# Kernel optimization log

Measured on AMD Instinct MI355X. Metric: run time of the kernel, lower is better.

The kernel has to match this reference:

```python
import jax, jax.numpy as jnp
import numpy as np

N, E, F_IN, H, C = 10000, 640000, 128, 128, 40


def setup_inputs() -> dict:
    key = jax.random.key(0)
    ks = jax.random.split(key, 8)
    x = jax.random.normal(ks[0], (N, F_IN), dtype=jnp.float32)
    edge_index = jax.random.randint(ks[1], (2, E), 0, N, dtype=jnp.int64)
    W1 = jax.random.normal(ks[2], (F_IN, H), dtype=jnp.float32) / np.sqrt(F_IN)
    b1 = jnp.zeros((H,), dtype=jnp.float32)
    W2 = jax.random.normal(ks[3], (H, H), dtype=jnp.float32) / np.sqrt(H)
    b2 = jnp.zeros((H,), dtype=jnp.float32)
    Wc = jax.random.normal(ks[4], (H, C), dtype=jnp.float32) / np.sqrt(H)
    bc = jnp.zeros((C,), dtype=jnp.float32)
    return {"x": x, "edge_index": edge_index, "W1": W1, "b1": b1,
            "W2": W2, "b2": b2, "Wc": Wc, "bc": bc}


def _gcn_conv(x, src, dst, norm, W, b):
    # GCNConv: out = D^{-1/2}(A+I)D^{-1/2} (x @ W) + b
    h = x @ W                               # [N, H]
    msg = h[src] * norm[:, None]            # gather + per-edge normalize
    out = jax.ops.segment_sum(msg, dst, num_segments=N)  # scatter-add
    return out + b


def reference(x, edge_index, W1, b1, W2, b2, Wc, bc):
    # add self-loops (as PyG GCNConv does by default)
    loops = jnp.arange(N, dtype=edge_index.dtype)
    src = jnp.concatenate([edge_index[0], loops])   # [E+N]
    dst = jnp.concatenate([edge_index[1], loops])   # [E+N]
    # symmetric normalization deg^{-1/2} with self-loops included
    deg = jax.ops.segment_sum(jnp.ones_like(dst, dtype=x.dtype), dst, num_segments=N)
    dinv = jax.lax.rsqrt(deg)                       # deg >= 1 due to self-loops
    norm = dinv[src] * dinv[dst]                    # [E+N]

    h = _gcn_conv(x, src, dst, norm, W1, b1)
    h = jax.nn.relu(h)
    h = _gcn_conv(h, src, dst, norm, W2, b2)
    logits = h @ Wc + bc                            # [N, C]
    return jax.nn.log_softmax(logits, axis=1)
```

## Files before the change

kernel.cpp:

```cpp
#include <hip/hip_runtime.h>
#include <hip/hip_fp16.h>
#include <math.h>

#define FDIM 128
#define CDIM 40
#define DMAX 192
#define NMAX 10240
#define SLICE_SHIFT 14
#define SLICE_SZ (1 << SLICE_SHIFT)

__device__ __forceinline__ uint2 pack_half4(float4 v) {
    __half2 p0 = __float22half2_rn(make_float2(v.x, v.y));
    __half2 p1 = __float22half2_rn(make_float2(v.z, v.w));
    uint2 u;
    u.x = *(unsigned int*)&p0;
    u.y = *(unsigned int*)&p1;
    return u;
}

__device__ __forceinline__ void unpack_add4(float acc[8], uint4 r) {
    __half2* p = (__half2*)&r;
    #pragma unroll
    for (int q = 0; q < 4; ++q) {
        float2 f = __half22float2(p[q]);
        acc[2 * q]     += f.x;
        acc[2 * q + 1] += f.y;
    }
}

__global__ __launch_bounds__(256) void k_hist(
        const int* __restrict__ dst, unsigned short* __restrict__ lrank,
        int* __restrict__ cnt, int e, int n) {
    __shared__ int h[NMAX];
    int tid = threadIdx.x;
    for (int i = tid; i < n; i += 256) h[i] = 0;
    __syncthreads();
    int base = (int)blockIdx.x << SLICE_SHIFT;
    int end = base + SLICE_SZ; if (end > e) end = e;
    for (int i = base + tid * 4; i < end; i += 1024) {
        if (i + 3 < end) {
            int4 d = *(const int4*)(dst + i);
            int p0 = atomicAdd(&h[d.x], 1);
            int p1 = atomicAdd(&h[d.y], 1);
            int p2 = atomicAdd(&h[d.z], 1);
            int p3 = atomicAdd(&h[d.w], 1);
            ushort4 r;
            r.x = (unsigned short)p0; r.y = (unsigned short)p1;
            r.z = (unsigned short)p2; r.w = (unsigned short)p3;
            *(ushort4*)(lrank + i) = r;
        } else {
            for (int k = i; k < end; ++k)
                lrank[k] = (unsigned short)atomicAdd(&h[dst[k]], 1);
        }
    }
    __syncthreads();
    int* c = cnt + (size_t)blockIdx.x * n;
    for (int i = tid; i < n; i += 256) c[i] = h[i];
}

__global__ __launch_bounds__(256) void k_scan(
        int* __restrict__ cnt, int* __restrict__ deg, int nslice, int n) {
    int v = blockIdx.x * 256 + threadIdx.x;
    if (v >= n) return;
    int s = 0;
    for (int b = 0; b < nslice; ++b) {
        int t = cnt[(size_t)b * n + v];
        cnt[(size_t)b * n + v] = s;
        s += t;
    }
    deg[v] = s;
}

__global__ __launch_bounds__(256) void k_mega(
        const float* __restrict__ A, const float* __restrict__ W,
        const int* __restrict__ deg, uint2* __restrict__ h16, int n,
        const int* __restrict__ src, const int* __restrict__ dst,
        const unsigned short* __restrict__ lrank, const int* __restrict__ base,
        unsigned short* __restrict__ col, int e, int gemm_blocks) {
    __shared__ float As[32][FDIM];
    int tid = threadIdx.x;
    if ((int)blockIdx.x < gemm_blocks) {
        int r0 = blockIdx.x * 32;
        for (int t = tid; t < 32 * 32; t += 256) {
            int r = t >> 5, c4 = t & 31;
            int gr = r0 + r;
            float4 v = make_float4(0.f, 0.f, 0.f, 0.f);
            if (gr < n) v = ((const float4*)A)[(size_t)gr * 32 + c4];
            ((float4*)As[r])[c4] = v;
        }
        __syncthreads();
        int cb = (tid & 31) * 4;
        int rb = (tid >> 5) * 4;
        float4 acc0 = make_float4(0,0,0,0), acc1 = acc0, acc2 = acc0, acc3 = acc0;
        for (int k = 0; k < FDIM; ++k) {
            float4 w = *(const float4*)(W + k * FDIM + cb);
            float a0 = As[rb + 0][k], a1 = As[rb + 1][k];
            float a2 = As[rb + 2][k], a3 = As[rb + 3][k];
            acc0.x += a0 * w.x; acc0.y += a0 * w.y; acc0.z += a0 * w.z; acc0.w += a0 * w.w;
            acc1.x += a1 * w.x; acc1.y += a1 * w.y; acc1.z += a1 * w.z; acc1.w += a1 * w.w;
            acc2.x += a2 * w.x; acc2.y += a2 * w.y; acc2.z += a2 * w.z; acc2.w += a2 * w.w;
            acc3.x += a3 * w.x; acc3.y += a3 * w.y; acc3.z += a3 * w.z; acc3.w += a3 * w.w;
        }
        float4 accs[4] = {acc0, acc1, acc2, acc3};
        #pragma unroll
        for (int i = 0; i < 4; ++i) {
            int gr = r0 + rb + i;
            if (gr < n) {
                float dinv = rsqrtf((float)(deg[gr] + 1));
                float4 v = accs[i];
                v.x *= dinv; v.y *= dinv; v.z *= dinv; v.w *= dinv;
                h16[(size_t)gr * 32 + (cb >> 2)] = pack_half4(v);
            }
        }
    } else {
        int t = ((int)blockIdx.x - gemm_blocks) * 256 + tid;
        int i8 = t * 8;
        if (i8 + 7 < e) {
            const int* bs = base + (size_t)(i8 >> SLICE_SHIFT) * n;
            int4 dA = ((const int4*)dst)[2 * t + 0];
            int4 dB = ((const int4*)dst)[2 * t + 1];
            int4 sA = ((const int4*)src)[2 * t + 0];
            int4 sB = ((const int4*)src)[2 * t + 1];
            ushort4 lA = ((const ushort4*)lrank)[2 * t + 0];
            ushort4 lB = ((const ushort4*)lrank)[2 * t + 1];
            int p0 = bs[dA.x] + lA.x;
            int p1 = bs[dA.y] + lA.y;
            int p2 = bs[dA.z] + lA.z;
            int p3 = bs[dA.w] + lA.w;
            int p4 = bs[dB.x] + lB.x;
            int p5 = bs[dB.y] + lB.y;
            int p6 = bs[dB.z] + lB.z;
            int p7 = bs[dB.w] + lB.w;
            if (p0 < DMAX) col[(size_t)dA.x * DMAX + p0] = (unsigned short)sA.x;
            if (p1 < DMAX) col[(size_t)dA.y * DMAX + p1] = (unsigned short)sA.y;
            if (p2 < DMAX) col[(size_t)dA.z * DMAX + p2] = (unsigned short)sA.z;
            if (p3 < DMAX) col[(size_t)dA.w * DMAX + p3] = (unsigned short)sA.w;
            if (p4 < DMAX) col[(size_t)dB.x * DMAX + p4] = (unsigned short)sB.x;
            if (p5 < DMAX) col[(size_t)dB.y * DMAX + p5] = (unsigned short)sB.y;
            if (p6 < DMAX) col[(size_t)dB.z * DMAX + p6] = (unsigned short)sB.z;
            if (p7 < DMAX) col[(size_t)dB.w * DMAX + p7] = (unsigned short)sB.w;
        } else if (i8 < e) {
            for (int k = i8; k < e; ++k) {
                int d = dst[k];
                int p = base[(size_t)(k >> SLICE_SHIFT) * n + d] + lrank[k];
                if (p < DMAX) col[(size_t)d * DMAX + p] = (unsigned short)src[k];
            }
        }
    }
}

template <bool RELU>
__device__ __forceinline__ void agg_gather(
        float out8[8], const uint4* __restrict__ hs,
        const unsigned short* __restrict__ col, const int* __restrict__ deg,
        const float* __restrict__ bias, int node, int l) {
    int dn = deg[node];
    float dinv = rsqrtf((float)(dn + 1));
    if (dn > DMAX) dn = DMAX;
    const uint4* cl8 = (const uint4*)(col + (size_t)node * DMAX);
    float a0[8], a1[8];
    #pragma unroll
    for (int q = 0; q < 8; ++q) { a0[q] = 0.f; a1[q] = 0.f; }
    unpack_add4(a0, hs[(size_t)node * 16 + l]);
    int nfull = dn >> 3;
    if (nfull > 0) {
        uint4 cc = cl8[0];
        for (int c = 0; c < nfull; ++c) {
            int cnext = (c + 1 < nfull) ? (c + 1) : c;
            uint4 cn = cl8[cnext];
            int s0 = cc.x & 0xFFFF, s1 = cc.x >> 16;
            int s2 = cc.y & 0xFFFF, s3 = cc.y >> 16;
            int s4 = cc.z & 0xFFFF, s5 = cc.z >> 16;
            int s6 = cc.w & 0xFFFF, s7 = cc.w >> 16;
            uint4 q0 = hs[(size_t)s0 * 16 + l];
            uint4 q1 = hs[(size_t)s1 * 16 + l];
            uint4 q2 = hs[(size_t)s2 * 16 + l];
            uint4 q3 = hs[(size_t)s3 * 16 + l];
            uint4 q4 = hs[(size_t)s4 * 16 + l];
            uint4 q5 = hs[(size_t)s5 * 16 + l];
            uint4 q6 = hs[(size_t)s6 * 16 + l];
            uint4 q7 = hs[(size_t)s7 * 16 + l];
            unpack_add4(a0, q0); unpack_add4(a1, q1);
            unpack_add4(a0, q2); unpack_add4(a1, q3);
            unpack_add4(a0, q4); unpack_add4(a1, q5);
            unpack_add4(a0, q6); unpack_add4(a1, q7);
            cc = cn;
        }
    }
    const unsigned short* cl = col + (size_t)node * DMAX;
    for (int j = nfull << 3; j < dn; ++j)
        unpack_add4(a0, hs[(size_t)cl[j] * 16 + l]);
    float4 b0 = ((const float4*)bias)[2 * l];
    float4 b1 = ((const float4*)bias)[2 * l + 1];
    float bb[8] = {b0.x, b0.y, b0.z, b0.w, b1.x, b1.y, b1.z, b1.w};
    #pragma unroll
    for (int q = 0; q < 8; ++q) {
        float v = dinv * (a0[q] + a1[q]) + bb[q];
        out8[q] = RELU ? fmaxf(v, 0.f) : v;
    }
}

__global__ __launch_bounds__(128) void k_agg_gemm(
        const uint4* __restrict__ hs1, const unsigned short* __restrict__ col,
        const int* __restrict__ deg, const float* __restrict__ b1,
        const float* __restrict__ W2, uint2* __restrict__ hs2, int n) {
    __shared__ float As[8][FDIM + 4];
    __shared__ float dl[8];
    int tid = threadIdx.x;
    int grp = tid >> 4, l = tid & 15;
    int node = blockIdx.x * 8 + grp;
    if (node < n) {
        float r8[8];
        agg_gather<true>(r8, hs1, col, deg, b1, node, l);
        float4* dst4 = (float4*)&As[grp][8 * l];
        dst4[0] = make_float4(r8[0], r8[1], r8[2], r8[3]);
        dst4[1] = make_float4(r8[4], r8[5], r8[6], r8[7]);
        if (l == 0) dl[grp] = rsqrtf((float)(deg[node] + 1));
    }
    __syncthreads();
    int cb = (tid & 31) * 4;
    int rb = (tid >> 5) * 2;
    float4 acc0 = make_float4(0,0,0,0), acc1 = acc0;
    for (int k = 0; k < FDIM; ++k) {
        float4 w = *(const float4*)(W2 + k * FDIM + cb);
        float x0 = As[rb][k], x1 = As[rb + 1][k];
        acc0.x += x0 * w.x; acc0.y += x0 * w.y; acc0.z += x0 * w.z; acc0.w += x0 * w.w;
        acc1.x += x1 * w.x; acc1.y += x1 * w.y; acc1.z += x1 * w.z; acc1.w += x1 * w.w;
    }
    int g0 = blockIdx.x * 8 + rb;
    if (g0 < n) {
        float s = dl[rb];
        float4 v = acc0;
        v.x *= s; v.y *= s; v.z *= s; v.w *= s;
        hs2[(size_t)g0 * 32 + (cb >> 2)] = pack_half4(v);
    }
    if (g0 + 1 < n) {
        float s = dl[rb + 1];
        float4 v = acc1;
        v.x *= s; v.y *= s; v.z *= s; v.w *= s;
        hs2[(size_t)(g0 + 1) * 32 + (cb >> 2)] = pack_half4(v);
    }
}

__global__ __launch_bounds__(128) void k_agg_cls(
        const uint4* __restrict__ hs2, const unsigned short* __restrict__ col,
        const int* __restrict__ deg, const float* __restrict__ b2,
        const float* __restrict__ Wc, const float* __restrict__ bc,
        float* __restrict__ out, int n) {
    __shared__ float As[8][FDIM + 4];
    int tid = threadIdx.x;
    int grp = tid >> 4, l = tid & 15;
    int node = blockIdx.x * 8 + grp;
    if (node < n) {
        float r8[8];
        agg_gather<false>(r8, hs2, col, deg, b2, node, l);
        float4* dst4 = (float4*)&As[grp][8 * l];
        dst4[0] = make_float4(r8[0], r8[1], r8[2], r8[3]);
        dst4[1] = make_float4(r8[4], r8[5], r8[6], r8[7]);
    }
    __syncthreads();
    int wv = tid >> 6, lane = tid & 63;
    #pragma unroll
    for (int ii = 0; ii < 4; ++ii) {
        int li = wv * 4 + ii;
        int nd = blockIdx.x * 8 + li;
        if (nd >= n) continue;
        const float* row = As[li];
        int c = (lane < CDIM) ? lane : (lane - 24);
        float acc = bc[c];
        for (int k = 0; k < FDIM; k += 4) {
            float a0 = row[k + 0], a1 = row[k + 1];
            float a2 = row[k + 2], a3 = row[k + 3];
            acc += a0 * Wc[(k + 0) * CDIM + c];
            acc += a1 * Wc[(k + 1) * CDIM + c];
            acc += a2 * Wc[(k + 2) * CDIM + c];
            acc += a3 * Wc[(k + 3) * CDIM + c];
        }
        float lv = (lane < CDIM) ? acc : -INFINITY;
        float m = lv;
        for (int off = 32; off > 0; off >>= 1) m = fmaxf(m, __shfl_down(m, off));
        m = __shfl(m, 0);
        float e = (lane < CDIM) ? expf(lv - m) : 0.0f;
        float s = e;
        for (int off = 32; off > 0; off >>= 1) s += __shfl_down(s, off);
        s = __shfl(s, 0);
        if (lane < CDIM) out[(size_t)nd * CDIM + lane] = lv - m - logf(s);
    }
}


extern "C" void kernel_launch(void* const* d_in, const int* in_sizes, int n_in,
                              void* d_out, int out_size, void* d_ws, size_t ws_size,
                              hipStream_t stream) {
    const float* x  = (const float*)d_in[0];
    const int*   ei = (const int*)d_in[1];
    const float* W1 = (const float*)d_in[2];
    const float* b1 = (const float*)d_in[3];
    const float* W2 = (const float*)d_in[4];
    const float* b2 = (const float*)d_in[5];
    const float* Wc = (const float*)d_in[6];
    const float* bc = (const float*)d_in[7];
    float* out = (float*)d_out;

    const int N = in_sizes[0] / FDIM;
    const int E = in_sizes[1] / 2;
    const int* srcp = ei;
    const int* dstp = ei + E;
    const int NSLICE = (E + SLICE_SZ - 1) >> SLICE_SHIFT;

    char* ws = (char*)d_ws;
    auto alloc = [&](size_t bytes) {
        char* p = ws;
        ws += (bytes + 255) & ~(size_t)255;
        return p;
    };
    int*            deg   = (int*)           alloc((size_t)N * 4);
    int*            cnt   = (int*)           alloc((size_t)NSLICE * N * 4);
    unsigned short* lrank = (unsigned short*)alloc((size_t)E * 2);
    unsigned short* col   = (unsigned short*)alloc((size_t)N * DMAX * 2);
    uint4*          h1h   = (uint4*)         alloc((size_t)N * 256);
    uint4*          h2h   = (uint4*)         alloc((size_t)N * 256);

    k_hist<<<NSLICE, 256, 0, stream>>>(dstp, lrank, cnt, E, N);

    k_scan<<<(N + 255) / 256, 256, 0, stream>>>(cnt, deg, NSLICE, N);

    int gb = (N + 31) / 32;
    int fb = (E / 8 + 255) / 256;
    k_mega<<<gb + fb, 256, 0, stream>>>(
        x, W1, deg, (uint2*)h1h, N, srcp, dstp, lrank, cnt, col, E, gb);

    k_agg_gemm<<<(N + 7) / 8, 128, 0, stream>>>(
        h1h, col, deg, b1, W2, (uint2*)h2h, N);

    k_agg_cls<<<(N + 7) / 8, 128, 0, stream>>>(
        h2h, col, deg, b2, Wc, bc, out, N);
}
```

Before: 161.9 us.

## Partition CSR fill by destination row range per XCD-aligned block group

```diff
diff --git a/kernel.cpp b/kernel.cpp
--- a/kernel.cpp
+++ b/kernel.cpp
@@ -76,7 +76,7 @@
         const int* __restrict__ deg, uint2* __restrict__ h16, int n,
         const int* __restrict__ src, const int* __restrict__ dst,
         const unsigned short* __restrict__ lrank, const int* __restrict__ base,
-        unsigned short* __restrict__ col, int e, int gemm_blocks) {
+        unsigned short* __restrict__ col, int e, int gemm_blocks, int eper) {
     __shared__ float As[32][FDIM];
     int tid = threadIdx.x;
     if ((int)blockIdx.x < gemm_blocks) {
@@ -113,37 +113,38 @@
             }
         }
     } else {
-        int t = ((int)blockIdx.x - gemm_blocks) * 256 + tid;
-        int i8 = t * 8;
-        if (i8 + 7 < e) {
-            const int* bs = base + (size_t)(i8 >> SLICE_SHIFT) * n;
-            int4 dA = ((const int4*)dst)[2 * t + 0];
-            int4 dB = ((const int4*)dst)[2 * t + 1];
-            int4 sA = ((const int4*)src)[2 * t + 0];
-            int4 sB = ((const int4*)src)[2 * t + 1];
-            ushort4 lA = ((const ushort4*)lrank)[2 * t + 0];
-            ushort4 lB = ((const ushort4*)lrank)[2 * t + 1];
-            int p0 = bs[dA.x] + lA.x;
-            int p1 = bs[dA.y] + lA.y;
-            int p2 = bs[dA.z] + lA.z;
-            int p3 = bs[dA.w] + lA.w;
-            int p4 = bs[dB.x] + lB.x;
-            int p5 = bs[dB.y] + lB.y;
-            int p6 = bs[dB.z] + lB.z;
-            int p7 = bs[dB.w] + lB.w;
-            if (p0 < DMAX) col[(size_t)dA.x * DMAX + p0] = (unsigned short)sA.x;
-            if (p1 < DMAX) col[(size_t)dA.y * DMAX + p1] = (unsigned short)sA.y;
-            if (p2 < DMAX) col[(size_t)dA.z * DMAX + p2] = (unsigned short)sA.z;
-            if (p3 < DMAX) col[(size_t)dA.w * DMAX + p3] = (unsigned short)sA.w;
-            if (p4 < DMAX) col[(size_t)dB.x * DMAX + p4] = (unsigned short)sB.x;
-            if (p5 < DMAX) col[(size_t)dB.y * DMAX + p5] = (unsigned short)sB.y;
-            if (p6 < DMAX) col[(size_t)dB.z * DMAX + p6] = (unsigned short)sB.z;
-            if (p7 < DMAX) col[(size_t)dB.w * DMAX + p7] = (unsigned short)sB.w;
-        } else if (i8 < e) {
-            for (int k = i8; k < e; ++k) {
-                int d = dst[k];
-                int p = base[(size_t)(k >> SLICE_SHIFT) * n + d] + lrank[k];
-                if (p < DMAX) col[(size_t)d * DMAX + p] = (unsigned short)src[k];
+        int fidx = (int)blockIdx.x - gemm_blocks;
+        int g = (int)(blockIdx.x & 7);
+        int j = fidx >> 3;
+        int rspan = (n + 7) >> 3;
+        int r_lo = g * rspan;
+        int r_hi = r_lo + rspan; if (r_hi > n) r_hi = n;
+        int beg = j * eper;
+        int end = beg + eper; if (end > e) end = e;
+        for (int i = beg + tid * 4; i < end; i += 1024) {
+            if (i + 3 < end) {
+                int4 d = *(const int4*)(dst + i);
+                bool m0 = (d.x >= r_lo) & (d.x < r_hi);
+                bool m1 = (d.y >= r_lo) & (d.y < r_hi);
+                bool m2 = (d.z >= r_lo) & (d.z < r_hi);
+                bool m3 = (d.w >= r_lo) & (d.w < r_hi);
+                if (m0 | m1 | m2 | m3) {
+                    int4 s = *(const int4*)(src + i);
+                    ushort4 lr = *(const ushort4*)(lrank + i);
+                    const int* bs = base + (size_t)(i >> SLICE_SHIFT) * n;
+                    if (m0) { int p = bs[d.x] + lr.x; if (p < DMAX) col[(size_t)d.x * DMAX + p] = (unsigned short)s.x; }
+                    if (m1) { int p = bs[d.y] + lr.y; if (p < DMAX) col[(size_t)d.y * DMAX + p] = (unsigned short)s.y; }
+                    if (m2) { int p = bs[d.z] + lr.z; if (p < DMAX) col[(size_t)d.z * DMAX + p] = (unsigned short)s.z; }
+                    if (m3) { int p = bs[d.w] + lr.w; if (p < DMAX) col[(size_t)d.w * DMAX + p] = (unsigned short)s.w; }
+                }
+            } else {
+                for (int k = i; k < end; ++k) {
+                    int d = dst[k];
+                    if (d >= r_lo && d < r_hi) {
+                        int p = base[(size_t)(k >> SLICE_SHIFT) * n + d] + lrank[k];
+                        if (p < DMAX) col[(size_t)d * DMAX + p] = (unsigned short)src[k];
+                    }
+                }
             }
         }
     }
@@ -326,9 +327,11 @@
     k_scan<<<(N + 255) / 256, 256, 0, stream>>>(cnt, deg, NSLICE, N);
 
     int gb = (N + 31) / 32;
-    int fb = (E / 8 + 255) / 256;
+    const int nbg = 40;
+    int eper = ((E + nbg - 1) / nbg + 3) & ~3;
+    int fb = nbg * 8;
     k_mega<<<gb + fb, 256, 0, stream>>>(
-        x, W1, deg, (uint2*)h1h, N, srcp, dstp, lrank, cnt, col, E, gb);
+        x, W1, deg, (uint2*)h1h, N, srcp, dstp, lrank, cnt, col, E, gb, eper);
 
     k_agg_gemm<<<(N + 7) / 8, 128, 0, stream>>>(
         h1h, col, deg, b1, W2, (uint2*)h2h, N);
```

Result: slower. 173.8 us (+7.3%).
